# Kernel tuning notes

Measured on AMD Instinct MI355X. Metric: run time of the kernel, lower is better.

Reference implementation:

```python
import jax, jax.numpy as jnp
import numpy as np

B, K, D_IN, H, CTX, RH = 4096, 4, 1024, 1024, 256, 64
TEMP, MIN_MOD = 1.0, 2
LN_EPS = 1e-5


def setup_inputs() -> dict:
    key = jax.random.key(0)
    ks = jax.random.split(key, 8)
    nrm = lambda i, shape, scale: jax.random.normal(ks[i], shape, jnp.float32) * scale
    return {
        "context": jax.random.normal(ks[0], (B, CTX), jnp.float32),
        "x": jax.random.normal(ks[1], (K, B, D_IN), jnp.float32),  # stacked modality inputs
        # Gumbel noise, matching -log(-log(U + 1e-8) + 1e-8)
        "gumbel": -jnp.log(-jnp.log(jax.random.uniform(ks[2], (B, K), jnp.float32) + 1e-8) + 1e-8),
        # router MLP params
        "W1": nrm(3, (CTX, RH), 1.0 / np.sqrt(CTX)), "b1": jnp.zeros((RH,), jnp.float32),
        "g_ln": jnp.ones((RH,), jnp.float32), "beta_ln": jnp.zeros((RH,), jnp.float32),
        "W2": nrm(4, (RH, RH // 2), 1.0 / np.sqrt(RH)), "b2": jnp.zeros((RH // 2,), jnp.float32),
        "W3": nrm(5, (RH // 2, K), 1.0 / np.sqrt(RH // 2)), "b3": jnp.zeros((K,), jnp.float32),
        "prior": jnp.zeros((K,), jnp.float32),
        # per-modality linear encoders (stacked)
        "W_enc": nrm(6, (K, D_IN, H), 1.0 / np.sqrt(D_IN)), "b_enc": jnp.zeros((K, H), jnp.float32),
        "fusion_w": jnp.ones((K,), jnp.float32),
    }


def reference(context, x, gumbel, W1, b1, g_ln, beta_ln, W2, b2, W3, b3,
              prior, W_enc, b_enc, fusion_w):
    # --- router MLP: Linear -> LayerNorm -> ReLU -> Linear -> ReLU -> Linear ---
    h = context @ W1 + b1                                   # [B, RH]
    mu = h.mean(-1, keepdims=True)
    var = h.var(-1, keepdims=True)
    h = (h - mu) / jnp.sqrt(var + LN_EPS) * g_ln + beta_ln
    h = jax.nn.relu(h)
    h = jax.nn.relu(h @ W2 + b2)                            # [B, RH//2]
    logits = h @ W3 + b3 + prior                            # [B, K]
    probs = jax.nn.sigmoid(logits)
    # Gumbel-sigmoid soft selection (training path)
    soft = jax.nn.sigmoid((logits + gumbel) / TEMP)
    # force top-min_modalities on
    _, top_idx = jax.lax.top_k(probs, MIN_MOD)              # [B, MIN_MOD]
    rows = jnp.arange(probs.shape[0])[:, None]
    min_mask = jnp.zeros_like(probs).at[rows, top_idx].set(1.0)
    mask = jnp.maximum(soft, min_mask)                      # [B, K]
    # --- conditional encoders: run only where mask > 0.5 (equiv: compute + zero) ---
    enc = jnp.einsum('kbd,kdh->bkh', x, W_enc) + b_enc[None, :, :]   # [B, K, H]
    hard = (mask > 0.5).astype(enc.dtype)                   # gather/scatter indicator
    enc = enc * hard[..., None] * mask[..., None]           # zero-fill + soft gating
    # --- fusion (softmax-weighted sum over modalities) ---
    w = jax.nn.softmax(fusion_w)                            # [K]
    fused = jnp.einsum('bkh,k->bh', enc, w)                 # [B, H]
    return fused
```

## Files before the change

kernel.cpp:

```cpp
#include <hip/hip_runtime.h>
#include <hip/hip_bf16.h>

#define NB    4096
#define NK    4
#define ND    1024
#define NH    1024
#define NCTX  256
#define NRH   64

typedef float f32x4 __attribute__((ext_vector_type(4)));
typedef float f32x8 __attribute__((ext_vector_type(8)));
typedef short s16x8 __attribute__((ext_vector_type(8)));
typedef _Float16 f16x8 __attribute__((ext_vector_type(8)));

__device__ __forceinline__ void gl_lds16(const void* g, void* l) {
    __builtin_amdgcn_global_load_lds(
        (const __attribute__((address_space(1))) unsigned int*)g,
        (__attribute__((address_space(3))) unsigned int*)l, 16, 0, 0);
}

__global__ __launch_bounds__(256) void router_k(
    const float* __restrict__ ctx, const float* __restrict__ gum,
    const float* __restrict__ W1, const float* __restrict__ b1,
    const float* __restrict__ gln, const float* __restrict__ bln,
    const float* __restrict__ W2, const float* __restrict__ b2,
    const float* __restrict__ W3, const float* __restrict__ b3,
    const float* __restrict__ prior, const float* __restrict__ fw,
    float* __restrict__ gates)
{
    __shared__ float sH[4][4][64];
    __shared__ float sH2[4][4][32];

    const int tid  = threadIdx.x;
    const int w    = tid >> 6;
    const int lane = tid & 63;
    const int rowbase = blockIdx.x * 16 + w * 4;
    const int rbu = __builtin_amdgcn_readfirstlane(rowbase);
    const float* c0 = ctx + (size_t)rbu * NCTX;

    float a0 = 0.f, a1 = 0.f, a2 = 0.f, a3 = 0.f;
#pragma unroll 8
    for (int d = 0; d < NCTX; ++d) {
        float wv = W1[d * NRH + lane];
        a0 = fmaf(c0[d],          wv, a0);
        a1 = fmaf(c0[NCTX + d],   wv, a1);
        a2 = fmaf(c0[2*NCTX + d], wv, a2);
        a3 = fmaf(c0[3*NCTX + d], wv, a3);
    }
    const float bb = b1[lane];
    float hr[4] = {a0 + bb, a1 + bb, a2 + bb, a3 + bb};
    const float gl = gln[lane], be = bln[lane];

#pragma unroll
    for (int r = 0; r < 4; ++r) {
        float h = hr[r];
        float s = h;
#pragma unroll
        for (int m = 32; m >= 1; m >>= 1) s += __shfl_xor(s, m);
        float mu = s * (1.f / 64.f);
        float dd = h - mu;
        float q = dd * dd;
#pragma unroll
        for (int m = 32; m >= 1; m >>= 1) q += __shfl_xor(q, m);
        float var = q * (1.f / 64.f);
        h = dd * rsqrtf(var + 1e-5f) * gl + be;
        sH[w][r][lane] = fmaxf(h, 0.f);
    }

#pragma unroll
    for (int p = 0; p < 2; ++p) {
        const int r = p * 2 + (lane >> 5);
        const int j = lane & 31;
        float acc = b2[j];
#pragma unroll 8
        for (int l = 0; l < 64; ++l)
            acc = fmaf(sH[w][r][l], W2[l * 32 + j], acc);
        sH2[w][r][j] = fmaxf(acc, 0.f);
    }

    const int r3 = lane >> 2, j3 = lane & 3;
    float lg = 0.f;
    if (lane < 16) {
        lg = b3[j3] + prior[j3];
#pragma unroll 8
        for (int l = 0; l < 32; ++l)
            lg = fmaf(sH2[w][r3][l], W3[l * 4 + j3], lg);
    }
    float pj = 1.f / (1.f + expf(-lg));
    const int base = lane & 60;
    float P0 = __shfl(pj, base), P1 = __shfl(pj, base | 1);
    float P2 = __shfl(pj, base | 2), P3 = __shfl(pj, base | 3);

    if (lane < 16) {
        float f0 = fw[0], f1 = fw[1], f2 = fw[2], f3 = fw[3];
        float fm = fmaxf(fmaxf(f0, f1), fmaxf(f2, f3));
        float e0 = expf(f0 - fm), e1 = expf(f1 - fm), e2 = expf(f2 - fm), e3 = expf(f3 - fm);
        float es = e0 + e1 + e2 + e3;
        float wsm = (j3 == 0 ? e0 : j3 == 1 ? e1 : j3 == 2 ? e2 : e3) / es;

        int cnt = 0;
        cnt += (P0 > pj) || ((P0 == pj) && (0 < j3));
        cnt += (P1 > pj) || ((P1 == pj) && (1 < j3));
        cnt += (P2 > pj) || ((P2 == pj) && (2 < j3));
        cnt += (P3 > pj) || ((P3 == pj) && (3 < j3));

        const int row = rowbase + r3;
        float soft = 1.f / (1.f + expf(-(lg + gum[row * 4 + j3])));
        float mask = (cnt < 2) ? 1.0f : soft;
        float gate = (mask > 0.5f) ? mask * wsm : 0.0f;
        gates[row * 4 + j3] = gate;
    }
}

__global__ __launch_bounds__(256) void wprep_k(
    const float* __restrict__ W, unsigned short* __restrict__ whi)
{
    __shared__ float sT[32][33];
    const int bid = blockIdx.x;
    const int k  = bid >> 10;
    const int dt = (bid >> 5) & 31;
    const int ht = bid & 31;
    const int t = threadIdx.x;
    {
        const int r  = t >> 3;
        const int c4 = (t & 7) << 2;
        const float* src = W + ((size_t)k << 20) + (size_t)(dt * 32 + r) * 1024 + (ht * 32 + c4);
        float4 v = *(const float4*)src;
        sT[c4 + 0][r] = v.x; sT[c4 + 1][r] = v.y;
        sT[c4 + 2][r] = v.z; sT[c4 + 3][r] = v.w;
    }
    __syncthreads();
    {
        const int h  = t >> 3;
        const int d4 = (t & 7) << 2;
        unsigned short uh[4];
#pragma unroll
        for (int q = 0; q < 4; ++q) {
            _Float16 hi = (_Float16)sT[h][d4 + q];
            uh[q] = __builtin_bit_cast(unsigned short, hi);
        }
        size_t o = ((size_t)k << 20) + (size_t)(ht * 32 + h) * 1024 + (dt * 32 + d4);
        *(ushort4*)(whi + o) = make_ushort4(uh[0], uh[1], uh[2], uh[3]);
    }
}

__global__ __launch_bounds__(256) void aprep_k(
    const float* __restrict__ x, const float* __restrict__ gates,
    unsigned short* __restrict__ Ah)
{
    const int bid = blockIdx.x;
    const int k  = bid >> 11;
    const int bp = bid & 2047;
    const int t = threadIdx.x;
    const int boff = t >> 7;
    const int d8 = (t & 127) << 3;
    const int b = bp * 2 + boff;
    const float g = gates[b * 4 + k];

    f32x8 v = *(const f32x8*)(x + ((size_t)k << 22) + (size_t)b * ND + d8);
    v *= g;
    f16x8 hb = __builtin_convertvector(v, f16x8);
    const size_t o = (size_t)b * 4096 + (k << 10) + d8;
    *(s16x8*)(Ah + o) = __builtin_bit_cast(s16x8, hb);
}

__global__ __launch_bounds__(256) void zero_k(float* __restrict__ out)
{
    const size_t i = ((size_t)blockIdx.x * 256 + threadIdx.x) * 8;
    *(f32x8*)(out + i) = (f32x8){0.f,0.f,0.f,0.f,0.f,0.f,0.f,0.f};
}

__global__ __launch_bounds__(256, 2) void gemm_k(
    const unsigned short* __restrict__ Ahg,
    const unsigned short* __restrict__ Bhg,
    const float* __restrict__ gates, const float* __restrict__ benc,
    float* __restrict__ out)
{
    __shared__ unsigned short sA[128 * 64];
    __shared__ unsigned short sB[128 * 64];

    const int bid = blockIdx.x;
    const int wg  = (bid & 7) * 64 + (bid >> 3);
    const int ksp = wg >> 8;
    const int rem = wg & 255;
    const int bm  = rem >> 3;
    const int bn  = rem & 7;

    const int tid = threadIdx.x;
    const int wv  = tid >> 6, ln = tid & 63;
    const int wr  = wv >> 1,  wc = wv & 1;
    const int l15 = ln & 15,  ls = ln >> 4;
    const int rowb = bm * 128;
    const int colb = bn * 128;

    const int srow = ln >> 3;
    const int slot = (ln & 7) ^ srow;
    size_t aoff[4], boff[4];
#pragma unroll
    for (int i = 0; i < 4; ++i) {
        const int row = (wv * 4 + i) * 8 + srow;
        aoff[i] = (size_t)(rowb + row) * 4096 + slot * 8;
        boff[i] = (size_t)(colb + row) * 1024 + slot * 8;
    }

    const int arow0 = (wr * 64 + l15) * 128;
    const int brow0 = (wc * 64 + l15) * 128;
    const int xr = (l15 & 7) << 4;
    int colswz[2];
#pragma unroll
    for (int kk = 0; kk < 2; ++kk)
        colswz[kk] = ((kk << 6) + (ls << 4)) ^ xr;

    f32x4 acc[4][4];
#pragma unroll
    for (int a = 0; a < 4; ++a)
#pragma unroll
        for (int b = 0; b < 4; ++b)
            acc[a][b] = (f32x4){0.f, 0.f, 0.f, 0.f};

#pragma unroll 1
    for (int kt = 0; kt < 32; ++kt) {
        const int kflat = ksp * 2048 + kt * 64;
        const size_t wk = ((size_t)(kflat >> 10) << 20) + (size_t)(kflat & 1023);

#pragma unroll
        for (int i = 0; i < 4; ++i) {
            const int chunk = wv * 4 + i;
            gl_lds16(Ahg + aoff[i] + kflat, &sA[chunk * 512]);
            gl_lds16(Bhg + boff[i] + wk,    &sB[chunk * 512]);
        }
        __syncthreads();

#pragma unroll
        for (int kk = 0; kk < 2; ++kk) {
            f16x8 af[4], bf[4];
#pragma unroll
            for (int mi = 0; mi < 4; ++mi)
                af[mi] = __builtin_bit_cast(f16x8,
                    *(const s16x8*)((const char*)sA + arow0 + mi * 2048 + colswz[kk]));
#pragma unroll
            for (int ni = 0; ni < 4; ++ni)
                bf[ni] = __builtin_bit_cast(f16x8,
                    *(const s16x8*)((const char*)sB + brow0 + ni * 2048 + colswz[kk]));
#pragma unroll
            for (int mi = 0; mi < 4; ++mi)
#pragma unroll
                for (int ni = 0; ni < 4; ++ni)
                    acc[mi][ni] = __builtin_amdgcn_mfma_f32_16x16x32_f16(
                        af[mi], bf[ni], acc[mi][ni], 0, 0, 0);
        }
        __syncthreads();
    }

    float bce[4][4];
    if (ksp == 0) {
#pragma unroll
        for (int ni = 0; ni < 4; ++ni) {
            const int col = colb + wc * 64 + ni * 16 + l15;
#pragma unroll
            for (int kk = 0; kk < 4; ++kk)
                bce[ni][kk] = benc[kk * NH + col];
        }
    }
#pragma unroll
    for (int mi = 0; mi < 4; ++mi) {
#pragma unroll
        for (int j = 0; j < 4; ++j) {
            const int row = rowb + wr * 64 + mi * 16 + ls * 4 + j;
            const float4 g = *(const float4*)(gates + row * 4);
#pragma unroll
            for (int ni = 0; ni < 4; ++ni) {
                const int col = colb + wc * 64 + ni * 16 + l15;
                float val = acc[mi][ni][j];
                if (ksp == 0)
                    val += g.x * bce[ni][0] + g.y * bce[ni][1] +
                           g.z * bce[ni][2] + g.w * bce[ni][3];
                unsafeAtomicAdd(out + (size_t)row * NH + col, val);
            }
        }
    }
}

extern "C" void kernel_launch(void* const* d_in, const int* in_sizes, int n_in,
                              void* d_out, int out_size, void* d_ws, size_t ws_size,
                              hipStream_t stream)
{
    const float* ctx   = (const float*)d_in[0];
    const float* x     = (const float*)d_in[1];
    const float* gum   = (const float*)d_in[2];
    const float* W1    = (const float*)d_in[3];
    const float* b1    = (const float*)d_in[4];
    const float* gln   = (const float*)d_in[5];
    const float* bln   = (const float*)d_in[6];
    const float* W2    = (const float*)d_in[7];
    const float* b2    = (const float*)d_in[8];
    const float* W3    = (const float*)d_in[9];
    const float* b3    = (const float*)d_in[10];
    const float* prior = (const float*)d_in[11];
    const float* Wenc  = (const float*)d_in[12];
    const float* benc  = (const float*)d_in[13];
    const float* fw    = (const float*)d_in[14];
    float* out = (float*)d_out;

    char* ws = (char*)d_ws;
    float* gates        = (float*)ws;
    unsigned short* bh  = (unsigned short*)(ws + (64 << 10));
    unsigned short* ah  = (unsigned short*)(ws + (64 << 10) + (8ull << 20));

    hipLaunchKernelGGL(router_k, dim3(256), dim3(256), 0, stream,
                       ctx, gum, W1, b1, gln, bln, W2, b2, W3, b3, prior, fw, gates);
    hipLaunchKernelGGL(aprep_k, dim3(8192), dim3(256), 0, stream, x, gates, ah);
    hipLaunchKernelGGL(wprep_k, dim3(4096), dim3(256), 0, stream, Wenc, bh);
    hipLaunchKernelGGL(zero_k, dim3(2048), dim3(256), 0, stream, out);
    hipLaunchKernelGGL(gemm_k, dim3(512), dim3(256), 0, stream,
                       ah, bh, gates, benc, out);
}
```

Measured before the change: 231.3 us.

## Fuse activation gating and fp16 conversion into GEMM with double-buffered LDS

Removes the separate aprep kernel, which scaled x by the gates and wrote an fp16 copy to workspace. The GEMM now loads fp32 x straight from global memory into registers, applies the gate, converts to fp16 and writes swizzled LDS itself. Shared buffers are double-buffered so the next tile's loads overlap the current MFMA compute. This avoids a full write and reread of the A matrix, at the cost of reading fp32 (twice the bytes) inside the GEMM, more registers, and twice the LDS.

```diff
diff --git a/kernel.cpp b/kernel.cpp
--- a/kernel.cpp
+++ b/kernel.cpp
@@ -144,26 +144,6 @@
     }
 }
 
-__global__ __launch_bounds__(256) void aprep_k(
-    const float* __restrict__ x, const float* __restrict__ gates,
-    unsigned short* __restrict__ Ah)
-{
-    const int bid = blockIdx.x;
-    const int k  = bid >> 11;
-    const int bp = bid & 2047;
-    const int t = threadIdx.x;
-    const int boff = t >> 7;
-    const int d8 = (t & 127) << 3;
-    const int b = bp * 2 + boff;
-    const float g = gates[b * 4 + k];
-
-    f32x8 v = *(const f32x8*)(x + ((size_t)k << 22) + (size_t)b * ND + d8);
-    v *= g;
-    f16x8 hb = __builtin_convertvector(v, f16x8);
-    const size_t o = (size_t)b * 4096 + (k << 10) + d8;
-    *(s16x8*)(Ah + o) = __builtin_bit_cast(s16x8, hb);
-}
-
 __global__ __launch_bounds__(256) void zero_k(float* __restrict__ out)
 {
     const size_t i = ((size_t)blockIdx.x * 256 + threadIdx.x) * 8;
@@ -171,13 +151,13 @@
 }
 
 __global__ __launch_bounds__(256, 2) void gemm_k(
-    const unsigned short* __restrict__ Ahg,
+    const float* __restrict__ x,
     const unsigned short* __restrict__ Bhg,
     const float* __restrict__ gates, const float* __restrict__ benc,
     float* __restrict__ out)
 {
-    __shared__ unsigned short sA[128 * 64];
-    __shared__ unsigned short sB[128 * 64];
+    __shared__ unsigned short sA0[128 * 64], sA1[128 * 64];
+    __shared__ unsigned short sB0[128 * 64], sB1[128 * 64];
 
     const int bid = blockIdx.x;
     const int wg  = (bid & 7) * 64 + (bid >> 3);
@@ -193,13 +173,21 @@
     const int rowb = bm * 128;
     const int colb = bn * 128;
 
+    const int arow_t = tid >> 1;
+    const int acol_t = (tid & 1) * 32;
+    const float* xrow = x + (size_t)(rowb + arow_t) * ND + acol_t;
+    const float* grow = gates + (rowb + arow_t) * 4;
+    int awr[4];
+#pragma unroll
+    for (int i = 0; i < 4; ++i)
+        awr[i] = arow_t * 128 + (((acol_t * 2) + i * 16) ^ ((arow_t & 7) << 4));
+
     const int srow = ln >> 3;
     const int slot = (ln & 7) ^ srow;
-    size_t aoff[4], boff[4];
+    size_t boff[4];
 #pragma unroll
     for (int i = 0; i < 4; ++i) {
         const int row = (wv * 4 + i) * 8 + srow;
-        aoff[i] = (size_t)(rowb + row) * 4096 + slot * 8;
         boff[i] = (size_t)(colb + row) * 1024 + slot * 8;
     }
 
@@ -218,39 +206,85 @@
         for (int b = 0; b < 4; ++b)
             acc[a][b] = (f32x4){0.f, 0.f, 0.f, 0.f};
 
+#define ALOAD(P, KT)                                                          \
+    do {                                                                      \
+        const int kf_ = ksp * 2048 + (KT) * 64;                               \
+        const int ks_ = kf_ >> 10, db_ = kf_ & 1023;                          \
+        const float* xp_ = xrow + ((size_t)ks_ << 22) + db_;                  \
+        P##g = grow[ks_];                                                     \
+        P##0 = *(const f32x8*)(xp_);                                          \
+        P##1 = *(const f32x8*)(xp_ + 8);                                      \
+        P##2 = *(const f32x8*)(xp_ + 16);                                     \
+        P##3 = *(const f32x8*)(xp_ + 24);                                     \
+    } while (0)
+
+#define AWRITE(P, SA)                                                         \
+    do {                                                                      \
+        f16x8 h0_ = __builtin_convertvector(P##0 * P##g, f16x8);              \
+        f16x8 h1_ = __builtin_convertvector(P##1 * P##g, f16x8);              \
+        f16x8 h2_ = __builtin_convertvector(P##2 * P##g, f16x8);              \
+        f16x8 h3_ = __builtin_convertvector(P##3 * P##g, f16x8);              \
+        *(s16x8*)((char*)(SA) + awr[0]) = __builtin_bit_cast(s16x8, h0_);     \
+        *(s16x8*)((char*)(SA) + awr[1]) = __builtin_bit_cast(s16x8, h1_);     \
+        *(s16x8*)((char*)(SA) + awr[2]) = __builtin_bit_cast(s16x8, h2_);     \
+        *(s16x8*)((char*)(SA) + awr[3]) = __builtin_bit_cast(s16x8, h3_);     \
+    } while (0)
+
+#define BSTAGE(SB, KT)                                                        \
+    do {                                                                      \
+        const int kf_ = ksp * 2048 + (KT) * 64;                               \
+        const size_t wk_ = ((size_t)(kf_ >> 10) << 20) + (size_t)(kf_ & 1023);\
+        _Pragma("unroll")                                                     \
+        for (int i = 0; i < 4; ++i)                                           \
+            gl_lds16(Bhg + boff[i] + wk_, &(SB)[(wv * 4 + i) * 512]);         \
+    } while (0)
+
+#define COMPUTE(SA, SB)                                                       \
+    do {                                                                      \
+        _Pragma("unroll")                                                     \
+        for (int kk = 0; kk < 2; ++kk) {                                      \
+            f16x8 af[4], bf[4];                                               \
+            _Pragma("unroll")                                                 \
+            for (int mi = 0; mi < 4; ++mi)                                    \
+                af[mi] = __builtin_bit_cast(f16x8,                            \
+                    *(const s16x8*)((const char*)(SA) + arow0 + mi * 2048 + colswz[kk])); \
+            _Pragma("unroll")                                                 \
+            for (int ni = 0; ni < 4; ++ni)                                    \
+                bf[ni] = __builtin_bit_cast(f16x8,                            \
+                    *(const s16x8*)((const char*)(SB) + brow0 + ni * 2048 + colswz[kk])); \
+            _Pragma("unroll")                                                 \
+            for (int mi = 0; mi < 4; ++mi)                                    \
+                _Pragma("unroll")                                             \
+                for (int ni = 0; ni < 4; ++ni)                                \
+                    acc[mi][ni] = __builtin_amdgcn_mfma_f32_16x16x32_f16(     \
+                        af[mi], bf[ni], acc[mi][ni], 0, 0, 0);                \
+        }                                                                     \
+    } while (0)
+
+    float LAg; f32x8 LA0, LA1, LA2, LA3;
+    float LBg; f32x8 LB0, LB1, LB2, LB3;
+
+    ALOAD(LA, 0);
+    BSTAGE(sB0, 0);
+    AWRITE(LA, sA0);
+    __syncthreads();
+
 #pragma unroll 1
-    for (int kt = 0; kt < 32; ++kt) {
-        const int kflat = ksp * 2048 + kt * 64;
-        const size_t wk = ((size_t)(kflat >> 10) << 20) + (size_t)(kflat & 1023);
-
-#pragma unroll
-        for (int i = 0; i < 4; ++i) {
-            const int chunk = wv * 4 + i;
-            gl_lds16(Ahg + aoff[i] + kflat, &sA[chunk * 512]);
-            gl_lds16(Bhg + boff[i] + wk,    &sB[chunk * 512]);
-        }
+    for (int kt = 0; kt < 32; kt += 2) {
+        ALOAD(LA, kt + 1);
+        BSTAGE(sB1, kt + 1);
+        COMPUTE(sA0, sB0);
+        AWRITE(LA, sA1);
         __syncthreads();
-
-#pragma unroll
-        for (int kk = 0; kk < 2; ++kk) {
-            f16x8 af[4], bf[4];
-#pragma unroll
-            for (int mi = 0; mi < 4; ++mi)
-                af[mi] = __builtin_bit_cast(f16x8,
-                    *(const s16x8*)((const char*)sA + arow0 + mi * 2048 + colswz[kk]));
-#pragma unroll
-            for (int ni = 0; ni < 4; ++ni)
-                bf[ni] = __builtin_bit_cast(f16x8,
-                    *(const s16x8*)((const char*)sB + brow0 + ni * 2048 + colswz[kk]));
-#pragma unroll
-            for (int mi = 0; mi < 4; ++mi)
-#pragma unroll
-                for (int ni = 0; ni < 4; ++ni)
-                    acc[mi][ni] = __builtin_amdgcn_mfma_f32_16x16x32_f16(
-                        af[mi], bf[ni], acc[mi][ni], 0, 0, 0);
-        }
+        if (kt + 2 < 32) { ALOAD(LB, kt + 2); BSTAGE(sB0, kt + 2); }
+        COMPUTE(sA1, sB1);
+        if (kt + 2 < 32) AWRITE(LB, sA0);
         __syncthreads();
     }
+#undef ALOAD
+#undef AWRITE
+#undef BSTAGE
+#undef COMPUTE
 
     float bce[4][4];
     if (ksp == 0) {
@@ -305,13 +339,11 @@
     char* ws = (char*)d_ws;
     float* gates        = (float*)ws;
     unsigned short* bh  = (unsigned short*)(ws + (64 << 10));
-    unsigned short* ah  = (unsigned short*)(ws + (64 << 10) + (8ull << 20));
 
     hipLaunchKernelGGL(router_k, dim3(256), dim3(256), 0, stream,
                        ctx, gum, W1, b1, gln, bln, W2, b2, W3, b3, prior, fw, gates);
-    hipLaunchKernelGGL(aprep_k, dim3(8192), dim3(256), 0, stream, x, gates, ah);
     hipLaunchKernelGGL(wprep_k, dim3(4096), dim3(256), 0, stream, Wenc, bh);
     hipLaunchKernelGGL(zero_k, dim3(2048), dim3(256), 0, stream, out);
     hipLaunchKernelGGL(gemm_k, dim3(512), dim3(256), 0, stream,
-                       ah, bh, gates, benc, out);
-}
+                       x, bh, gates, benc, out);
+}
```

New measurement: 262.1 us. 13.3% more time.
